# Optimization experiments

Measured on AMD Instinct MI355X. Metric: run time of the kernel, lower is better.

## Reference

```python
import jax, jax.numpy as jnp
import numpy as np

HIDDEN = 1024
HEADS = 16
HEAD_DIM = HIDDEN // HEADS


def setup_inputs() -> dict:
    key = jax.random.key(0)
    ks = jax.random.split(key, 8)
    B, S = 2, 2048
    scale = 1.0 / np.sqrt(HIDDEN)
    inp = {
        "hidden_states": jax.random.normal(ks[0], (B, S, HIDDEN), dtype=jnp.float32),
        "attention_mask": jnp.zeros((B, 1, 1, S), dtype=jnp.float32),
        "q_w": jax.random.normal(ks[1], (HIDDEN, HIDDEN), dtype=jnp.float32) * scale,
        "q_b": jnp.zeros((HIDDEN,), dtype=jnp.float32),
        "k_w": jax.random.normal(ks[2], (HIDDEN, HIDDEN), dtype=jnp.float32) * scale,
        "k_b": jnp.zeros((HIDDEN,), dtype=jnp.float32),
        "v_w": jax.random.normal(ks[3], (HIDDEN, HIDDEN), dtype=jnp.float32) * scale,
        "v_b": jnp.zeros((HIDDEN,), dtype=jnp.float32),
    }
    return inp


def _split_heads(x):
    # [B, S, H] -> [B, heads, S, head_dim]
    B, S, _ = x.shape
    return x.reshape(B, S, HEADS, HEAD_DIM).transpose(0, 2, 1, 3)


def reference(hidden_states, attention_mask, q_w, q_b, k_w, k_b, v_w, v_b):
    # Linear projections (torch Linear: x @ W.T + b; here weights stored as [in, out])
    q = _split_heads(hidden_states @ q_w + q_b)  # [B, h, S, d]
    k = _split_heads(hidden_states @ k_w + k_b)
    v = _split_heads(hidden_states @ v_w + v_b)

    scores = jnp.einsum("bhqd,bhkd->bhqk", q, k) / jnp.sqrt(jnp.float32(HEAD_DIM))
    scores = scores + attention_mask  # additive mask, broadcast [B,1,1,S]
    probs = jax.nn.softmax(scores, axis=-1)
    # dropout prob = 0.0 -> identity
    ctx = jnp.einsum("bhqk,bhkd->bhqd", probs, v)  # [B, h, S, d]
    B, _, S, _ = ctx.shape
    ctx = ctx.transpose(0, 2, 1, 3).reshape(B, S, HIDDEN)
    return ctx
```

## Files before the change

### kernel.cpp

```cpp
#include <hip/hip_runtime.h>

typedef __bf16 bf16;
typedef __attribute__((ext_vector_type(8))) __bf16 bf16x8;
typedef __attribute__((ext_vector_type(4))) __bf16 bf16x4;
typedef __attribute__((ext_vector_type(4))) float f32x4;

#define MFMA(a, b, c) __builtin_amdgcn_mfma_f32_16x16x32_bf16((a), (b), (c), 0, 0, 0)
#define LOG2E 1.44269504088896340736f

__device__ __forceinline__ bf16x8 cvt8(float4 a, float4 b) {
  bf16x8 r;
  r[0] = (bf16)a.x; r[1] = (bf16)a.y; r[2] = (bf16)a.z; r[3] = (bf16)a.w;
  r[4] = (bf16)b.x; r[5] = (bf16)b.y; r[6] = (bf16)b.z; r[7] = (bf16)b.w;
  return r;
}

__device__ __forceinline__ void stage16(const bf16* g, bf16* l) {
  __builtin_amdgcn_global_load_lds(
      (const __attribute__((address_space(1))) void*)g,
      (__attribute__((address_space(3))) void*)l, 16, 0, 0);
}

__global__ __launch_bounds__(256)
void cvt(const float* __restrict__ hs, const float* __restrict__ qw,
         const float* __restrict__ kw, const float* __restrict__ vw,
         bf16* __restrict__ Xb, bf16* __restrict__ Wt) {
  const int bid = blockIdx.x, tid = threadIdx.x;
  if (bid < 2048) {
    size_t off = (size_t)bid * 2048 + tid * 8;
    float4 x0 = *(const float4*)(hs + off);
    float4 x1 = *(const float4*)(hs + off + 4);
    *(bf16x8*)(Xb + off) = cvt8(x0, x1);
  } else {
    int t = bid - 2048;
    int z = t >> 8, ti = t & 255;
    const float* W = (z == 0) ? qw : (z == 1) ? kw : vw;
    int k0 = (ti >> 4) * 64, n0 = (ti & 15) * 64;
    __shared__ bf16 T[64 * 72];
    #pragma unroll
    for (int i = 0; i < 16; ++i) {
      int e = i * 256 + tid;
      int kr = e >> 6, nc = e & 63;
      T[nc * 72 + kr] = (bf16)W[(size_t)(k0 + kr) * 1024 + n0 + nc];
    }
    __syncthreads();
    #pragma unroll
    for (int i = 0; i < 2; ++i) {
      int e = i * 256 + tid;
      int nr = e >> 3, kg = e & 7;
      *(bf16x8*)(Wt + (size_t)z * 1048576 + (size_t)(n0 + nr) * 1024 + k0 + kg * 8) =
          *(const bf16x8*)&T[nr * 72 + kg * 8];
    }
  }
}

__global__ __launch_bounds__(256)
void qkv_gemm(const bf16* __restrict__ Xb, const bf16* __restrict__ Wt,
              const float* __restrict__ qbias, const float* __restrict__ kbias,
              const float* __restrict__ vbias,
              bf16* __restrict__ qo, bf16* __restrict__ ko, bf16* __restrict__ vo) {
  const int nb = blockIdx.x;
  const int mb = blockIdx.y;
  const int z = nb >> 3, nbm = nb & 7;
  const bf16* W = Wt + (size_t)z * 1048576;

  const int tid = threadIdx.x;
  const int wave = tid >> 6, lane = tid & 63, quad = lane >> 4, c = lane & 15;
  const int wr = wave >> 1, wc = wave & 1;
  const int lrow = lane >> 3;
  const int lg = (lane & 7) ^ lrow;

  __shared__ bf16 As[128 * 64];
  __shared__ bf16 Bs[128 * 64];

  f32x4 acc[4][4] = {};

  for (int k0 = 0; k0 < 1024; k0 += 64) {
    #pragma unroll
    for (int i = 0; i < 4; ++i) {
      int r = wave * 32 + i * 8;
      stage16(Xb + (size_t)(mb * 128 + r + lrow) * 1024 + k0 + lg * 8, &As[r * 64]);
      stage16(W + (size_t)(nbm * 128 + r + lrow) * 1024 + k0 + lg * 8, &Bs[r * 64]);
    }
    __syncthreads();
    #pragma unroll
    for (int ch = 0; ch < 2; ++ch) {
      bf16x8 af[4];
      #pragma unroll
      for (int rt = 0; rt < 4; ++rt) {
        int row = wr * 64 + rt * 16 + c;
        af[rt] = *(const bf16x8*)&As[row * 64 + ((((ch << 2) | quad) ^ (c & 7)) << 3)];
      }
      #pragma unroll
      for (int nt = 0; nt < 4; ++nt) {
        int row = wc * 64 + nt * 16 + c;
        bf16x8 bfrag = *(const bf16x8*)&Bs[row * 64 + ((((ch << 2) | quad) ^ (c & 7)) << 3)];
        #pragma unroll
        for (int rt = 0; rt < 4; ++rt)
          acc[rt][nt] = MFMA(af[rt], bfrag, acc[rt][nt]);
      }
    }
    __syncthreads();
  }

  const float* bias = (z == 0) ? qbias : (z == 1) ? kbias : vbias;
  float bv[4];
  #pragma unroll
  for (int nt = 0; nt < 4; ++nt)
    bv[nt] = bias[nbm * 128 + wc * 64 + nt * 16 + c];

  if (z == 2) {
    #pragma unroll
    for (int rt = 0; rt < 4; ++rt)
      #pragma unroll
      for (int nt = 0; nt < 4; ++nt) {
        int m0 = mb * 128 + wr * 64 + rt * 16 + 4 * quad;
        int n = nbm * 128 + wc * 64 + nt * 16 + c;
        bf16x4 pk;
        #pragma unroll
        for (int reg = 0; reg < 4; ++reg) pk[reg] = (bf16)(acc[rt][nt][reg] + bv[nt]);
        int b = m0 >> 11, s0 = m0 & 2047, h = n >> 6, d = n & 63;
        *(bf16x4*)&vo[(((size_t)b * 16 + h) * 64 + d) * 2048 + s0] = pk;
      }
  } else {
    bf16* dst = (z == 0) ? qo : ko;
    const float scale = (z == 0) ? 0.125f * LOG2E : 1.0f;
    #pragma unroll
    for (int rt = 0; rt < 4; ++rt)
      #pragma unroll
      for (int nt = 0; nt < 4; ++nt)
        #pragma unroll
        for (int reg = 0; reg < 4; ++reg) {
          float v = (acc[rt][nt][reg] + bv[nt]) * scale;
          int m = mb * 128 + wr * 64 + rt * 16 + 4 * quad + reg;
          int n = nbm * 128 + wc * 64 + nt * 16 + c;
          int b = m >> 11, s = m & 2047, h = n >> 6, d = n & 63;
          dst[(((size_t)b * 16 + h) * 2048 + s) * 64 + d] = (bf16)v;
        }
  }
}

__global__ __launch_bounds__(256)
void attn(const bf16* __restrict__ qg, const bf16* __restrict__ kg,
          const bf16* __restrict__ vtg, const float* __restrict__ mask,
          float* __restrict__ out) {
  const int qblk = blockIdx.x;
  const int bh = blockIdx.y;
  const int b = bh >> 4, h = bh & 15;
  const int tid = threadIdx.x;
  const int wave = tid >> 6, lane = tid & 63, quad = lane >> 4, c = lane & 15;
  const int lrow = lane >> 3, lg = (lane & 7) ^ lrow;

  __shared__ bf16 Ks[64 * 64];
  __shared__ bf16 Vs[64 * 64];
  __shared__ bf16 Ps[4][2048];

  const bf16* qb_ = qg + (size_t)bh * 2048 * 64;
  const bf16* kb_ = kg + (size_t)bh * 2048 * 64;
  const bf16* vb_ = vtg + (size_t)bh * 64 * 2048;

  bf16x8 qf[2][2];
  #pragma unroll
  for (int rt = 0; rt < 2; ++rt)
    #pragma unroll
    for (int ch = 0; ch < 2; ++ch)
      qf[rt][ch] = *(const bf16x8*)(qb_ +
          (size_t)(qblk * 128 + wave * 32 + rt * 16 + c) * 64 + ch * 32 + quad * 8);

  f32x4 o[2][4] = {};
  float lsum[2][4] = {};

  for (int kt = 0; kt < 32; ++kt) {
    #pragma unroll
    for (int i = 0; i < 2; ++i) {
      int r = wave * 16 + i * 8;
      stage16(kb_ + (size_t)(kt * 64 + r + lrow) * 64 + lg * 8, &Ks[r * 64]);
      stage16(vb_ + (size_t)(r + lrow) * 2048 + kt * 64 + lg * 8, &Vs[r * 64]);
    }
    __syncthreads();

    f32x4 s[2][4] = {};
    #pragma unroll
    for (int nt = 0; nt < 4; ++nt)
      #pragma unroll
      for (int ch = 0; ch < 2; ++ch) {
        bf16x8 kf = *(const bf16x8*)&Ks[(nt * 16 + c) * 64 +
                                        ((((ch << 2) | quad) ^ (c & 7)) << 3)];
        #pragma unroll
        for (int rt = 0; rt < 2; ++rt)
          s[rt][nt] = MFMA(qf[rt][ch], kf, s[rt][nt]);
      }

    float mv[4];
    #pragma unroll
    for (int nt = 0; nt < 4; ++nt)
      mv[nt] = mask[b * 2048 + kt * 64 + nt * 16 + c] * LOG2E;

    #pragma unroll
    for (int rt = 0; rt < 2; ++rt)
      #pragma unroll
      for (int nt = 0; nt < 4; ++nt)
        #pragma unroll
        for (int reg = 0; reg < 4; ++reg) {
          float p = __builtin_amdgcn_exp2f(s[rt][nt][reg] + mv[nt]);
          lsum[rt][reg] += p;
          int r = 4 * quad + reg;
          int gk = nt * 2 + (c >> 3);
          Ps[wave][rt * 1024 + r * 64 + ((gk ^ (r & 7)) << 3) + (c & 7)] = (bf16)p;
        }
    __asm__ volatile("s_waitcnt lgkmcnt(0)" ::: "memory");

    #pragma unroll
    for (int ch = 0; ch < 2; ++ch) {
      bf16x8 pa[2];
      #pragma unroll
      for (int rt = 0; rt < 2; ++rt)
        pa[rt] = *(const bf16x8*)&Ps[wave][rt * 1024 + c * 64 +
                                          ((((ch << 2) | quad) ^ (c & 7)) << 3)];
      #pragma unroll
      for (int nt = 0; nt < 4; ++nt) {
        bf16x8 vf = *(const bf16x8*)&Vs[(nt * 16 + c) * 64 +
                                        ((((ch << 2) | quad) ^ (c & 7)) << 3)];
        #pragma unroll
        for (int rt = 0; rt < 2; ++rt)
          o[rt][nt] = MFMA(pa[rt], vf, o[rt][nt]);
      }
    }
    __syncthreads();
  }

  #pragma unroll
  for (int rt = 0; rt < 2; ++rt)
    #pragma unroll
    for (int reg = 0; reg < 4; ++reg) {
      float l = lsum[rt][reg];
      #pragma unroll
      for (int off = 1; off < 16; off <<= 1) l += __shfl_xor(l, off, 64);
      float inv = 1.0f / l;
      int srow = qblk * 128 + wave * 32 + rt * 16 + 4 * quad + reg;
      #pragma unroll
      for (int nt = 0; nt < 4; ++nt)
        out[((size_t)b * 2048 + srow) * 1024 + h * 64 + nt * 16 + c] =
            o[rt][nt][reg] * inv;
    }
}

extern "C" void kernel_launch(void* const* d_in, const int* in_sizes, int n_in,
                              void* d_out, int out_size, void* d_ws, size_t ws_size,
                              hipStream_t stream) {
  const float* hs   = (const float*)d_in[0];
  const float* mask = (const float*)d_in[1];
  const float* qw   = (const float*)d_in[2];
  const float* qb   = (const float*)d_in[3];
  const float* kw   = (const float*)d_in[4];
  const float* kb   = (const float*)d_in[5];
  const float* vw   = (const float*)d_in[6];
  const float* vb   = (const float*)d_in[7];
  float* out = (float*)d_out;

  bf16* Xb   = (bf16*)d_ws;
  bf16* Wt   = Xb + (size_t)4096 * 1024;
  bf16* q_ws = Wt + (size_t)3 * 1048576;
  bf16* k_ws = q_ws + (size_t)4096 * 1024;
  bf16* v_ws = k_ws + (size_t)4096 * 1024;

  cvt<<<dim3(2816), 256, 0, stream>>>(hs, qw, kw, vw, Xb, Wt);
  qkv_gemm<<<dim3(24, 32), 256, 0, stream>>>(Xb, Wt, qb, kb, vb, q_ws, k_ws, v_ws);
  attn<<<dim3(16, 32), 256, 0, stream>>>(q_ws, k_ws, v_ws, mask, out);
}
```

Measured before the change: 187.3 us.

## Remap blocks to XCDs and split attention work across eight waves

Both the QKV GEMM and the attention kernel now use a 1D grid remapped so that consecutive tiles sharing the same rows or head land on the same XCD, which should improve L2 reuse of shared operands. The attention kernel moves from 4 waves handling 32 query rows each to 8 waves handling 16 rows each in a 512-thread block. This halves per-wave registers and raises wave-level parallelism, while K/V staging is spread over more waves. Launch bounds also add occupancy hints. In exchange, each K/V tile gets less reuse per wave and there is more barrier synchronisation per block.

```diff
diff --git a/kernel.cpp b/kernel.cpp
--- a/kernel.cpp
+++ b/kernel.cpp
@@ -54,13 +54,15 @@
   }
 }
 
-__global__ __launch_bounds__(256)
+__global__ __launch_bounds__(256, 3)
 void qkv_gemm(const bf16* __restrict__ Xb, const bf16* __restrict__ Wt,
               const float* __restrict__ qbias, const float* __restrict__ kbias,
               const float* __restrict__ vbias,
               bf16* __restrict__ qo, bf16* __restrict__ ko, bf16* __restrict__ vo) {
-  const int nb = blockIdx.x;
-  const int mb = blockIdx.y;
+  const int blk = blockIdx.x;
+  const int xcd = blk & 7, slot = blk >> 3;
+  const int mb = xcd * 4 + slot / 24;
+  const int nb = slot % 24;
   const int z = nb >> 3, nbm = nb & 7;
   const bf16* W = Wt + (size_t)z * 1048576;
 
@@ -140,12 +142,14 @@
   }
 }
 
-__global__ __launch_bounds__(256)
+__global__ __launch_bounds__(512, 4)
 void attn(const bf16* __restrict__ qg, const bf16* __restrict__ kg,
           const bf16* __restrict__ vtg, const float* __restrict__ mask,
           float* __restrict__ out) {
-  const int qblk = blockIdx.x;
-  const int bh = blockIdx.y;
+  const int blk = blockIdx.x;
+  const int xcd = blk & 7, slot = blk >> 3;
+  const int bh = xcd * 4 + (slot >> 4);
+  const int qblk = slot & 15;
   const int b = bh >> 4, h = bh & 15;
   const int tid = threadIdx.x;
   const int wave = tid >> 6, lane = tid & 63, quad = lane >> 4, c = lane & 15;
@@ -153,42 +157,37 @@
 
   __shared__ bf16 Ks[64 * 64];
   __shared__ bf16 Vs[64 * 64];
-  __shared__ bf16 Ps[4][2048];
+  __shared__ bf16 Ps[8][1024];
 
   const bf16* qb_ = qg + (size_t)bh * 2048 * 64;
   const bf16* kb_ = kg + (size_t)bh * 2048 * 64;
   const bf16* vb_ = vtg + (size_t)bh * 64 * 2048;
 
-  bf16x8 qf[2][2];
+  bf16x8 qf[2];
   #pragma unroll
-  for (int rt = 0; rt < 2; ++rt)
-    #pragma unroll
-    for (int ch = 0; ch < 2; ++ch)
-      qf[rt][ch] = *(const bf16x8*)(qb_ +
-          (size_t)(qblk * 128 + wave * 32 + rt * 16 + c) * 64 + ch * 32 + quad * 8);
-
-  f32x4 o[2][4] = {};
-  float lsum[2][4] = {};
+  for (int ch = 0; ch < 2; ++ch)
+    qf[ch] = *(const bf16x8*)(qb_ +
+        (size_t)(qblk * 128 + wave * 16 + c) * 64 + ch * 32 + quad * 8);
+
+  f32x4 o[4] = {};
+  float lsum[4] = {};
 
   for (int kt = 0; kt < 32; ++kt) {
-    #pragma unroll
-    for (int i = 0; i < 2; ++i) {
-      int r = wave * 16 + i * 8;
+    {
+      int r = wave * 8;
       stage16(kb_ + (size_t)(kt * 64 + r + lrow) * 64 + lg * 8, &Ks[r * 64]);
       stage16(vb_ + (size_t)(r + lrow) * 2048 + kt * 64 + lg * 8, &Vs[r * 64]);
     }
     __syncthreads();
 
-    f32x4 s[2][4] = {};
+    f32x4 s[4] = {};
     #pragma unroll
     for (int nt = 0; nt < 4; ++nt)
       #pragma unroll
       for (int ch = 0; ch < 2; ++ch) {
         bf16x8 kf = *(const bf16x8*)&Ks[(nt * 16 + c) * 64 +
                                         ((((ch << 2) | quad) ^ (c & 7)) << 3)];
-        #pragma unroll
-        for (int rt = 0; rt < 2; ++rt)
-          s[rt][nt] = MFMA(qf[rt][ch], kf, s[rt][nt]);
+        s[nt] = MFMA(qf[ch], kf, s[nt]);
       }
 
     float mv[4];
@@ -197,52 +196,43 @@
       mv[nt] = mask[b * 2048 + kt * 64 + nt * 16 + c] * LOG2E;
 
     #pragma unroll
-    for (int rt = 0; rt < 2; ++rt)
-      #pragma unroll
-      for (int nt = 0; nt < 4; ++nt)
-        #pragma unroll
-        for (int reg = 0; reg < 4; ++reg) {
-          float p = __builtin_amdgcn_exp2f(s[rt][nt][reg] + mv[nt]);
-          lsum[rt][reg] += p;
-          int r = 4 * quad + reg;
-          int gk = nt * 2 + (c >> 3);
-          Ps[wave][rt * 1024 + r * 64 + ((gk ^ (r & 7)) << 3) + (c & 7)] = (bf16)p;
-        }
+    for (int nt = 0; nt < 4; ++nt)
+      #pragma unroll
+      for (int reg = 0; reg < 4; ++reg) {
+        float p = __builtin_amdgcn_exp2f(s[nt][reg] + mv[nt]);
+        lsum[reg] += p;
+        int r = 4 * quad + reg;
+        int gk = nt * 2 + (c >> 3);
+        Ps[wave][r * 64 + ((gk ^ (r & 7)) << 3) + (c & 7)] = (bf16)p;
+      }
     __asm__ volatile("s_waitcnt lgkmcnt(0)" ::: "memory");
 
     #pragma unroll
     for (int ch = 0; ch < 2; ++ch) {
-      bf16x8 pa[2];
-      #pragma unroll
-      for (int rt = 0; rt < 2; ++rt)
-        pa[rt] = *(const bf16x8*)&Ps[wave][rt * 1024 + c * 64 +
-                                          ((((ch << 2) | quad) ^ (c & 7)) << 3)];
+      bf16x8 pa = *(const bf16x8*)&Ps[wave][c * 64 +
+                                           ((((ch << 2) | quad) ^ (c & 7)) << 3)];
       #pragma unroll
       for (int nt = 0; nt < 4; ++nt) {
         bf16x8 vf = *(const bf16x8*)&Vs[(nt * 16 + c) * 64 +
                                         ((((ch << 2) | quad) ^ (c & 7)) << 3)];
-        #pragma unroll
-        for (int rt = 0; rt < 2; ++rt)
-          o[rt][nt] = MFMA(pa[rt], vf, o[rt][nt]);
+        o[nt] = MFMA(pa, vf, o[nt]);
       }
     }
     __syncthreads();
   }
 
   #pragma unroll
-  for (int rt = 0; rt < 2; ++rt)
-    #pragma unroll
-    for (int reg = 0; reg < 4; ++reg) {
-      float l = lsum[rt][reg];
-      #pragma unroll
-      for (int off = 1; off < 16; off <<= 1) l += __shfl_xor(l, off, 64);
-      float inv = 1.0f / l;
-      int srow = qblk * 128 + wave * 32 + rt * 16 + 4 * quad + reg;
-      #pragma unroll
-      for (int nt = 0; nt < 4; ++nt)
-        out[((size_t)b * 2048 + srow) * 1024 + h * 64 + nt * 16 + c] =
-            o[rt][nt][reg] * inv;
-    }
+  for (int reg = 0; reg < 4; ++reg) {
+    float l = lsum[reg];
+    #pragma unroll
+    for (int off = 1; off < 16; off <<= 1) l += __shfl_xor(l, off, 64);
+    float inv = 1.0f / l;
+    int srow = qblk * 128 + wave * 16 + 4 * quad + reg;
+    #pragma unroll
+    for (int nt = 0; nt < 4; ++nt)
+      out[((size_t)b * 2048 + srow) * 1024 + h * 64 + nt * 16 + c] =
+          o[nt][reg] * inv;
+  }
 }
 
 extern "C" void kernel_launch(void* const* d_in, const int* in_sizes, int n_in,
@@ -265,6 +255,6 @@
   bf16* v_ws = k_ws + (size_t)4096 * 1024;
 
   cvt<<<dim3(2816), 256, 0, stream>>>(hs, qw, kw, vw, Xb, Wt);
-  qkv_gemm<<<dim3(24, 32), 256, 0, stream>>>(Xb, Wt, qb, kb, vb, q_ws, k_ws, v_ws);
-  attn<<<dim3(16, 32), 256, 0, stream>>>(q_ws, k_ws, v_ws, mask, out);
-}
+  qkv_gemm<<<dim3(768), 256, 0, stream>>>(Xb, Wt, qb, kb, vb, q_ws, k_ws, v_ws);
+  attn<<<dim3(512), 512, 0, stream>>>(q_ws, k_ws, v_ws, mask, out);
+}
```

Measured after the change: 178.6 us. -4.7%, faster.

## Double-buffer LDS staging in GEMM and attention, add XCD-aware block remapping

Applied to the files above, without the earlier changes.

Both the QKV GEMM and the attention kernel now use two LDS buffers, so the next K/V (or A/B) tile is prefetched with global_load_lds while the current one is consumed, and one barrier per iteration is removed. The GEMM K-step shrinks from 64 to 32 with a matching 4-group swizzle. Both grids become 1D with an XCD-aware remap so that blocks sharing inputs land on the same XCD and can reuse its L2. Launch bounds gain occupancy hints. The cost is extra LDS use and more loop iterations in the GEMM.

```diff
diff --git a/kernel.cpp b/kernel.cpp
--- a/kernel.cpp
+++ b/kernel.cpp
@@ -54,53 +54,66 @@
   }
 }
 
-__global__ __launch_bounds__(256)
+__global__ __launch_bounds__(256, 3)
 void qkv_gemm(const bf16* __restrict__ Xb, const bf16* __restrict__ Wt,
               const float* __restrict__ qbias, const float* __restrict__ kbias,
               const float* __restrict__ vbias,
               bf16* __restrict__ qo, bf16* __restrict__ ko, bf16* __restrict__ vo) {
-  const int nb = blockIdx.x;
-  const int mb = blockIdx.y;
+  const int blk = blockIdx.x;
+  const int xcd = blk & 7, slot = blk >> 3;
+  const int mb = xcd * 4 + slot / 24;
+  const int nb = slot % 24;
   const int z = nb >> 3, nbm = nb & 7;
   const bf16* W = Wt + (size_t)z * 1048576;
 
   const int tid = threadIdx.x;
   const int wave = tid >> 6, lane = tid & 63, quad = lane >> 4, c = lane & 15;
   const int wr = wave >> 1, wc = wave & 1;
-  const int lrow = lane >> 3;
-  const int lg = (lane & 7) ^ lrow;
-
-  __shared__ bf16 As[128 * 64];
-  __shared__ bf16 Bs[128 * 64];
+  const int r4 = lane >> 2;
+  const int g4 = (lane & 3) ^ (r4 & 3);
+
+  __shared__ bf16 As[2][128 * 32];
+  __shared__ bf16 Bs[2][128 * 32];
+
+  const bf16* aS0 = Xb + (size_t)(mb * 128 + wave * 16 + r4) * 1024 + g4 * 8;
+  const bf16* aS1 = aS0 + (size_t)64 * 1024;
+  const bf16* bS0 = W + (size_t)(nbm * 128 + wave * 16 + r4) * 1024 + g4 * 8;
+  const bf16* bS1 = bS0 + (size_t)64 * 1024;
+  const int d0 = (wave * 16) * 32, d1 = (64 + wave * 16) * 32;
+
+  int aOff[4], bOff[4];
+  #pragma unroll
+  for (int t = 0; t < 4; ++t) {
+    aOff[t] = (wr * 64 + t * 16 + c) * 32 + ((quad ^ (c & 3)) << 3);
+    bOff[t] = (wc * 64 + t * 16 + c) * 32 + ((quad ^ (c & 3)) << 3);
+  }
 
   f32x4 acc[4][4] = {};
 
-  for (int k0 = 0; k0 < 1024; k0 += 64) {
-    #pragma unroll
-    for (int i = 0; i < 4; ++i) {
-      int r = wave * 32 + i * 8;
-      stage16(Xb + (size_t)(mb * 128 + r + lrow) * 1024 + k0 + lg * 8, &As[r * 64]);
-      stage16(W + (size_t)(nbm * 128 + r + lrow) * 1024 + k0 + lg * 8, &Bs[r * 64]);
-    }
+  stage16(aS0, &As[0][d0]);
+  stage16(aS1, &As[0][d1]);
+  stage16(bS0, &Bs[0][d0]);
+  stage16(bS1, &Bs[0][d1]);
+
+  for (int k0 = 0; k0 < 1024; k0 += 32) {
     __syncthreads();
-    #pragma unroll
-    for (int ch = 0; ch < 2; ++ch) {
-      bf16x8 af[4];
-      #pragma unroll
-      for (int rt = 0; rt < 4; ++rt) {
-        int row = wr * 64 + rt * 16 + c;
-        af[rt] = *(const bf16x8*)&As[row * 64 + ((((ch << 2) | quad) ^ (c & 7)) << 3)];
-      }
-      #pragma unroll
-      for (int nt = 0; nt < 4; ++nt) {
-        int row = wc * 64 + nt * 16 + c;
-        bf16x8 bfrag = *(const bf16x8*)&Bs[row * 64 + ((((ch << 2) | quad) ^ (c & 7)) << 3)];
-        #pragma unroll
-        for (int rt = 0; rt < 4; ++rt)
-          acc[rt][nt] = MFMA(af[rt], bfrag, acc[rt][nt]);
-      }
-    }
-    __syncthreads();
+    const int buf = (k0 >> 5) & 1;
+    if (k0 < 992) {
+      stage16(aS0 + k0 + 32, &As[buf ^ 1][d0]);
+      stage16(aS1 + k0 + 32, &As[buf ^ 1][d1]);
+      stage16(bS0 + k0 + 32, &Bs[buf ^ 1][d0]);
+      stage16(bS1 + k0 + 32, &Bs[buf ^ 1][d1]);
+    }
+    bf16x8 af[4];
+    #pragma unroll
+    for (int rt = 0; rt < 4; ++rt) af[rt] = *(const bf16x8*)&As[buf][aOff[rt]];
+    #pragma unroll
+    for (int nt = 0; nt < 4; ++nt) {
+      bf16x8 bfrag = *(const bf16x8*)&Bs[buf][bOff[nt]];
+      #pragma unroll
+      for (int rt = 0; rt < 4; ++rt)
+        acc[rt][nt] = MFMA(af[rt], bfrag, acc[rt][nt]);
+    }
   }
 
   const float* bias = (z == 0) ? qbias : (z == 1) ? kbias : vbias;
@@ -140,24 +153,27 @@
   }
 }
 
-__global__ __launch_bounds__(256)
+__global__ __launch_bounds__(256, 2)
 void attn(const bf16* __restrict__ qg, const bf16* __restrict__ kg,
           const bf16* __restrict__ vtg, const float* __restrict__ mask,
           float* __restrict__ out) {
-  const int qblk = blockIdx.x;
-  const int bh = blockIdx.y;
+  const int blk = blockIdx.x;
+  const int xcd = blk & 7, slot = blk >> 3;
+  const int bh = xcd * 4 + (slot >> 4);
+  const int qblk = slot & 15;
   const int b = bh >> 4, h = bh & 15;
   const int tid = threadIdx.x;
   const int wave = tid >> 6, lane = tid & 63, quad = lane >> 4, c = lane & 15;
   const int lrow = lane >> 3, lg = (lane & 7) ^ lrow;
 
-  __shared__ bf16 Ks[64 * 64];
-  __shared__ bf16 Vs[64 * 64];
+  __shared__ bf16 Ks[2][64 * 64];
+  __shared__ bf16 Vs[2][64 * 64];
   __shared__ bf16 Ps[4][2048];
 
   const bf16* qb_ = qg + (size_t)bh * 2048 * 64;
   const bf16* kb_ = kg + (size_t)bh * 2048 * 64;
   const bf16* vb_ = vtg + (size_t)bh * 64 * 2048;
+  const float* mk_ = mask + (size_t)b * 2048;
 
   bf16x8 qf[2][2];
   #pragma unroll
@@ -170,22 +186,36 @@
   f32x4 o[2][4] = {};
   float lsum[2][4] = {};
 
+  {
+    int r = wave * 16;
+    stage16(kb_ + (size_t)(r + lrow) * 64 + lg * 8, &Ks[0][r * 64]);
+    stage16(kb_ + (size_t)(r + 8 + lrow) * 64 + lg * 8, &Ks[0][(r + 8) * 64]);
+    stage16(vb_ + (size_t)(r + lrow) * 2048 + lg * 8, &Vs[0][r * 64]);
+    stage16(vb_ + (size_t)(r + 8 + lrow) * 2048 + lg * 8, &Vs[0][(r + 8) * 64]);
+  }
+
   for (int kt = 0; kt < 32; ++kt) {
-    #pragma unroll
-    for (int i = 0; i < 2; ++i) {
-      int r = wave * 16 + i * 8;
-      stage16(kb_ + (size_t)(kt * 64 + r + lrow) * 64 + lg * 8, &Ks[r * 64]);
-      stage16(vb_ + (size_t)(r + lrow) * 2048 + kt * 64 + lg * 8, &Vs[r * 64]);
-    }
     __syncthreads();
+    const int cur = kt & 1;
+    if (kt < 31) {
+      int r = wave * 16;
+      stage16(kb_ + (size_t)((kt + 1) * 64 + r + lrow) * 64 + lg * 8,
+              &Ks[cur ^ 1][r * 64]);
+      stage16(kb_ + (size_t)((kt + 1) * 64 + r + 8 + lrow) * 64 + lg * 8,
+              &Ks[cur ^ 1][(r + 8) * 64]);
+      stage16(vb_ + (size_t)(r + lrow) * 2048 + (kt + 1) * 64 + lg * 8,
+              &Vs[cur ^ 1][r * 64]);
+      stage16(vb_ + (size_t)(r + 8 + lrow) * 2048 + (kt + 1) * 64 + lg * 8,
+              &Vs[cur ^ 1][(r + 8) * 64]);
+    }
 
     f32x4 s[2][4] = {};
     #pragma unroll
     for (int nt = 0; nt < 4; ++nt)
       #pragma unroll
       for (int ch = 0; ch < 2; ++ch) {
-        bf16x8 kf = *(const bf16x8*)&Ks[(nt * 16 + c) * 64 +
-                                        ((((ch << 2) | quad) ^ (c & 7)) << 3)];
+        bf16x8 kf = *(const bf16x8*)&Ks[cur][(nt * 16 + c) * 64 +
+                                            ((((ch << 2) | quad) ^ (c & 7)) << 3)];
         #pragma unroll
         for (int rt = 0; rt < 2; ++rt)
           s[rt][nt] = MFMA(qf[rt][ch], kf, s[rt][nt]);
@@ -194,7 +224,7 @@
     float mv[4];
     #pragma unroll
     for (int nt = 0; nt < 4; ++nt)
-      mv[nt] = mask[b * 2048 + kt * 64 + nt * 16 + c] * LOG2E;
+      mv[nt] = mk_[kt * 64 + nt * 16 + c] * LOG2E;
 
     #pragma unroll
     for (int rt = 0; rt < 2; ++rt)
@@ -219,14 +249,13 @@
                                           ((((ch << 2) | quad) ^ (c & 7)) << 3)];
       #pragma unroll
       for (int nt = 0; nt < 4; ++nt) {
-        bf16x8 vf = *(const bf16x8*)&Vs[(nt * 16 + c) * 64 +
-                                        ((((ch << 2) | quad) ^ (c & 7)) << 3)];
+        bf16x8 vf = *(const bf16x8*)&Vs[cur][(nt * 16 + c) * 64 +
+                                            ((((ch << 2) | quad) ^ (c & 7)) << 3)];
         #pragma unroll
         for (int rt = 0; rt < 2; ++rt)
           o[rt][nt] = MFMA(pa[rt], vf, o[rt][nt]);
       }
     }
-    __syncthreads();
   }
 
   #pragma unroll
@@ -265,6 +294,6 @@
   bf16* v_ws = k_ws + (size_t)4096 * 1024;
 
   cvt<<<dim3(2816), 256, 0, stream>>>(hs, qw, kw, vw, Xb, Wt);
-  qkv_gemm<<<dim3(24, 32), 256, 0, stream>>>(Xb, Wt, qb, kb, vb, q_ws, k_ws, v_ws);
-  attn<<<dim3(16, 32), 256, 0, stream>>>(q_ws, k_ws, v_ws, mask, out);
-}
+  qkv_gemm<<<dim3(768), 256, 0, stream>>>(Xb, Wt, qb, kb, vb, q_ws, k_ws, v_ws);
+  attn<<<dim3(512), 256, 0, stream>>>(q_ws, k_ws, v_ws, mask, out);
+}
```

Measured after the change: 186.0 us. Within noise of the previous version (-0.7%).
